# Optimization experiments

Hardware: AMD Instinct MI355X
Metric: run time of the kernel (lower is better)

The kernel has to match this reference:

```python
import jax, jax.numpy as jnp
import numpy as np

LEAK = 0.1
BN_EPS = 1e-3  # keras BatchNormalization default epsilon
H = 256        # LSTM hidden size


def _conv1d_same(x, k):
    # x: [B, T, Cin], k: [3, Cin, Cout] -> [B, T, Cout]
    return jax.lax.conv_general_dilated(x, k, (1,), 'SAME',
                                        dimension_numbers=('NWC', 'WIO', 'NWC'))


def _bn_leaky(x, gamma, beta, mean, var):
    y = (x - mean) * jax.lax.rsqrt(var + BN_EPS) * gamma + beta
    return jnp.where(y > 0, y, LEAK * y)


def _lstm_cell(x, h, c, W, U, b):
    # keras LSTMCell: gates ordered i, f, g(candidate), o
    z = x @ W + h @ U + b  # [B, 4H]
    i, f, g, o = jnp.split(z, 4, axis=-1)
    c_new = jax.nn.sigmoid(f) * c + jax.nn.sigmoid(i) * jnp.tanh(g)
    h_new = jax.nn.sigmoid(o) * jnp.tanh(c_new)
    return h_new, c_new


def setup_inputs() -> dict:
    key = jax.random.key(0)
    ks = jax.random.split(key, 16)
    B, T = 128, 1024
    d = {}
    d['imu'] = jax.random.normal(ks[0], (B, T, 6), dtype=jnp.float32)
    # conv encoder params (no bias)
    chans = [(6, 64), (64, 128), (128, 256)]
    for li, (cin, cout) in enumerate(chans, start=1):
        d[f'k{li}'] = jax.random.normal(ks[li], (3, cin, cout), jnp.float32) * (1.0 / np.sqrt(3 * cin))
        d[f'g{li}'] = jnp.ones((cout,), jnp.float32)
        d[f'b{li}'] = jnp.zeros((cout,), jnp.float32)
        d[f'm{li}'] = jax.random.normal(ks[li + 3], (cout,), jnp.float32) * 0.05
        d[f'v{li}'] = jax.random.uniform(ks[li + 6], (cout,), jnp.float32) + 0.5
    # stacked LSTM params (2 layers of 256 units)
    for li, kidx in [(1, 10), (2, 13)]:
        d[f'W{li}'] = jax.random.normal(ks[kidx], (H, 4 * H), jnp.float32) * (1.0 / np.sqrt(H))
        d[f'U{li}'] = jax.random.normal(ks[kidx + 1], (H, 4 * H), jnp.float32) * (1.0 / np.sqrt(H))
        d[f'bl{li}'] = jnp.zeros((4 * H,), jnp.float32)
    return d


def reference(imu, k1, g1, b1, m1, v1, k2, g2, b2, m2, v2, k3, g3, b3, m3, v3,
              W1, U1, bl1, W2, U2, bl2):
    # Conv1D-BN-LeakyReLU encoder (inference-mode BN, training=False)
    x = _bn_leaky(_conv1d_same(imu, k1), g1, b1, m1, v1)
    x = _bn_leaky(_conv1d_same(x, k2), g2, b2, m2, v2)
    x = _bn_leaky(_conv1d_same(x, k3), g3, b3, m3, v3)   # [B, T, 256]

    B = x.shape[0]
    init = tuple(jnp.zeros((B, H), x.dtype) for _ in range(4))  # h1, c1, h2, c2

    def step(carry, xt):
        h1, c1, h2, c2 = carry
        h1, c1 = _lstm_cell(xt, h1, c1, W1, U1, bl1)
        h2, c2 = _lstm_cell(h1, h2, c2, W2, U2, bl2)
        return (h1, c1, h2, c2), h2

    xs = jnp.swapaxes(x, 0, 1)           # [T, B, 256]
    _, ys = jax.lax.scan(step, init, xs)  # ys: [T, B, 256] top-layer outputs
    return jnp.mean(ys, axis=0)           # global average pool over time -> [B, 256]
```

## Files before the change

kernel.cpp:

```cpp
#include <hip/hip_runtime.h>
#include <hip/hip_bf16.h>

#define T_SEQ 1024
#define NB 128
#define HID 256
#define TEAM_BLK 32

typedef __attribute__((ext_vector_type(8))) short short8;
typedef __attribute__((ext_vector_type(4))) float f32x4;

__device__ __forceinline__ unsigned short f2bf(float f) {
  unsigned int u = __builtin_bit_cast(unsigned int, f);
  unsigned int r = (u + 0x7fffu + ((u >> 16) & 1u)) >> 16;
  return (unsigned short)r;
}

__device__ __forceinline__ float sigm(float x) { return 1.0f / (1.0f + expf(-x)); }

__device__ __forceinline__ int swz(int r, int k) {
  return (((r << 10) + (k << 1)) ^ ((r & 7) << 4)) >> 1;
}

__device__ __forceinline__ short8 ld_h16(const unsigned short* p) {
  unsigned long long lo = __hip_atomic_load((const unsigned long long*)p,
                                            __ATOMIC_RELAXED, __HIP_MEMORY_SCOPE_AGENT);
  unsigned long long hi = __hip_atomic_load((const unsigned long long*)(p + 4),
                                            __ATOMIC_RELAXED, __HIP_MEMORY_SCOPE_AGENT);
  union { unsigned long long q[2]; short8 v; } u;
  u.q[0] = lo; u.q[1] = hi;
  return u.v;
}
__device__ __forceinline__ void st_h(unsigned short* p, unsigned short v) {
  __hip_atomic_store(p, v, __ATOMIC_RELAXED, __HIP_MEMORY_SCOPE_AGENT);
}

__device__ __forceinline__ void team_arrive(unsigned int* flags, int bid, unsigned int val) {
  asm volatile("s_waitcnt vmcnt(0) lgkmcnt(0)" ::: "memory");
  if (threadIdx.x == 0)
    __hip_atomic_store(flags + bid, val, __ATOMIC_RELAXED, __HIP_MEMORY_SCOPE_AGENT);
}
__device__ __forceinline__ void team_wait(const unsigned int* flags, unsigned int val) {
  const unsigned int* p = flags + (threadIdx.x & 31);
  for (;;) {
    unsigned int v = __hip_atomic_load(p, __ATOMIC_RELAXED, __HIP_MEMORY_SCOPE_AGENT);
    if (__all(v >= val)) break;
    __builtin_amdgcn_s_sleep(1);
  }
  asm volatile("" ::: "memory");
}


__global__ void conv1_kernel(const float* __restrict__ imu, const float* __restrict__ k1,
                             const float* __restrict__ g1, const float* __restrict__ b1,
                             const float* __restrict__ m1, const float* __restrict__ v1,
                             float* __restrict__ y1) {
  int idx = blockIdx.x * 256 + threadIdx.x;
  int c = idx & 63;
  int t = (idx >> 6) & (T_SEQ - 1);
  int b = idx >> 16;
  float acc = 0.f;
#pragma unroll
  for (int dt = 0; dt < 3; ++dt) {
    int tt = t + dt - 1;
    if (tt >= 0 && tt < T_SEQ) {
      const float* ip = imu + ((size_t)b * T_SEQ + tt) * 6;
#pragma unroll
      for (int ci = 0; ci < 6; ++ci)
        acc += ip[ci] * k1[(dt * 6 + ci) * 64 + c];
    }
  }
  float sc = g1[c] * rsqrtf(v1[c] + 1e-3f);
  float y = (acc - m1[c]) * sc + b1[c];
  y1[idx] = y > 0.f ? y : 0.1f * y;
}

__global__ __launch_bounds__(128) void conv2_kernel(
    const float* __restrict__ y1, const float* __restrict__ k2,
    const float* __restrict__ g2, const float* __restrict__ b2,
    const float* __restrict__ m2, const float* __restrict__ v2,
    float* __restrict__ y2) {
  __shared__ float yt[18 * 64];
  const int b = blockIdx.x >> 6;
  const int t0 = (blockIdx.x & 63) << 4;
  for (int i = threadIdx.x; i < 18 * 64; i += 128) {
    int r = i >> 6, ci = i & 63;
    int tt = t0 - 1 + r;
    yt[i] = (tt >= 0 && tt < T_SEQ) ? y1[((size_t)b * T_SEQ + tt) * 64 + ci] : 0.f;
  }
  __syncthreads();
  const int c = threadIdx.x;
  float acc[16];
#pragma unroll
  for (int u = 0; u < 16; ++u) acc[u] = 0.f;
  for (int ci = 0; ci < 64; ++ci) {
    float w0 = k2[(0 * 64 + ci) * 128 + c];
    float w1 = k2[(1 * 64 + ci) * 128 + c];
    float w2 = k2[(2 * 64 + ci) * 128 + c];
    float rv[18];
#pragma unroll
    for (int r = 0; r < 18; ++r) rv[r] = yt[r * 64 + ci];
#pragma unroll
    for (int u = 0; u < 16; ++u)
      acc[u] += rv[u] * w0 + rv[u + 1] * w1 + rv[u + 2] * w2;
  }
  float sc = g2[c] * rsqrtf(v2[c] + 1e-3f);
  float sh = b2[c] - m2[c] * sc;
#pragma unroll
  for (int u = 0; u < 16; ++u) {
    float y = acc[u] * sc + sh;
    y2[((size_t)b * T_SEQ + (t0 + u)) * 128 + c] = y > 0.f ? y : 0.1f * y;
  }
}

__global__ __launch_bounds__(128) void conv3_kernel(
    const float* __restrict__ y2, const float* __restrict__ k3,
    const float* __restrict__ g3, const float* __restrict__ b3,
    const float* __restrict__ m3, const float* __restrict__ v3,
    unsigned short* __restrict__ x) {
  __shared__ float yt[18 * 128];
  const int b = blockIdx.x >> 6;
  const int t0 = (blockIdx.x & 63) << 4;
  for (int i = threadIdx.x; i < 18 * 128; i += 128) {
    int r = i >> 7, ci = i & 127;
    int tt = t0 - 1 + r;
    yt[i] = (tt >= 0 && tt < T_SEQ) ? y2[((size_t)b * T_SEQ + tt) * 128 + ci] : 0.f;
  }
  __syncthreads();
  const int c0 = threadIdx.x;
  float acc0[16], acc1[16];
#pragma unroll
  for (int u = 0; u < 16; ++u) { acc0[u] = 0.f; acc1[u] = 0.f; }
  for (int ci = 0; ci < 128; ++ci) {
    float w00 = k3[(0 * 128 + ci) * 256 + c0];
    float w01 = k3[(1 * 128 + ci) * 256 + c0];
    float w02 = k3[(2 * 128 + ci) * 256 + c0];
    float w10 = k3[(0 * 128 + ci) * 256 + c0 + 128];
    float w11 = k3[(1 * 128 + ci) * 256 + c0 + 128];
    float w12 = k3[(2 * 128 + ci) * 256 + c0 + 128];
    float rv[18];
#pragma unroll
    for (int r = 0; r < 18; ++r) rv[r] = yt[r * 128 + ci];
#pragma unroll
    for (int u = 0; u < 16; ++u) {
      acc0[u] += rv[u] * w00 + rv[u + 1] * w01 + rv[u + 2] * w02;
      acc1[u] += rv[u] * w10 + rv[u + 1] * w11 + rv[u + 2] * w12;
    }
  }
  float sca = g3[c0] * rsqrtf(v3[c0] + 1e-3f);
  float sha = b3[c0] - m3[c0] * sca;
  float scb = g3[c0 + 128] * rsqrtf(v3[c0 + 128] + 1e-3f);
  float shb = b3[c0 + 128] - m3[c0 + 128] * scb;
#pragma unroll
  for (int u = 0; u < 16; ++u) {
    float ya = acc0[u] * sca + sha;
    float yb = acc1[u] * scb + shb;
    ya = ya > 0.f ? ya : 0.1f * ya;
    yb = yb > 0.f ? yb : 0.1f * yb;
    size_t base = ((size_t)(t0 + u) * NB + b) * HID;
    x[base + c0] = f2bf(ya);
    x[base + c0 + 128] = f2bf(yb);
  }
}


__global__ __launch_bounds__(64) void lstm_kernel(
    const unsigned short* __restrict__ x,
    const float* __restrict__ W1, const float* __restrict__ U1, const float* __restrict__ bl1,
    const float* __restrict__ W2, const float* __restrict__ U2, const float* __restrict__ bl2,
    unsigned short* __restrict__ hbufs,
    unsigned int* __restrict__ bars,
    float* __restrict__ out) {
  __shared__ unsigned short wt[64 * 512];

  const int team = blockIdx.x >> 5;
  const int bid = blockIdx.x & 31;
  const bool is_l2 = bid >= 16;
  const int j0 = (bid & 15) << 4;
  const int lane = threadIdx.x;
  const int b0 = team << 4;

  const float* Wx = is_l2 ? W2 : W1;
  const float* Wh = is_l2 ? U2 : U1;
  const float* bl = is_l2 ? bl2 : bl1;

  {
    const int r = lane;
    const int col = ((r >> 4) << 8) + j0 + (r & 15);
    for (int k0 = 0; k0 < 256; k0 += 8) {
      short8 sx, sh;
#pragma unroll
      for (int u = 0; u < 8; ++u) {
        sx[u] = (short)f2bf(Wx[(size_t)(k0 + u) * 1024 + col]);
        sh[u] = (short)f2bf(Wh[(size_t)(k0 + u) * 1024 + col]);
      }
      *(short8*)&wt[swz(r, k0)] = sx;
      *(short8*)&wt[swz(r, 256 + k0)] = sh;
    }
  }

  const int lo4 = lane & 15;
  const int klo = (lane >> 4) << 3;

  float bias[4];
#pragma unroll
  for (int g = 0; g < 4; ++g) bias[g] = bl[(g << 8) + j0 + lo4];

  unsigned short* h1buf = hbufs + (size_t)team * 16384;
  unsigned short* h2buf = h1buf + 8192;
  unsigned int* flags = bars + team * 64;

  float cst[4] = {0.f, 0.f, 0.f, 0.f};
  float oacc[4] = {0.f, 0.f, 0.f, 0.f};
  f32x4 acc[4];

  if (!is_l2) {
#pragma unroll
    for (int g = 0; g < 4; ++g) acc[g] = (f32x4){bias[g], bias[g], bias[g], bias[g]};
    const unsigned short* xs = x + (size_t)(b0 + lo4) * HID;
#pragma unroll
    for (int kk = 0; kk < 8; ++kk) {
      short8 a = *(const short8*)(xs + kk * 32 + klo);
#pragma unroll
      for (int g = 0; g < 4; ++g)
        acc[g] = __builtin_amdgcn_mfma_f32_16x16x32_bf16(
            a, *(const short8*)&wt[swz((g << 4) + lo4, (kk << 5) + klo)], acc[g], 0, 0, 0);
    }
  }

  for (int ph = 0; ph <= T_SEQ; ++ph) {
    if (!is_l2) {
      if (ph < T_SEQ) {
        const unsigned short* hs = h1buf + ((ph + 1) & 1) * 4096 + lo4 * 256;
        short8 av[8];
#pragma unroll
        for (int kk = 0; kk < 8; ++kk) av[kk] = ld_h16(hs + kk * 32 + klo);
#pragma unroll
        for (int kk = 0; kk < 8; ++kk)
#pragma unroll
          for (int g = 0; g < 4; ++g)
            acc[g] = __builtin_amdgcn_mfma_f32_16x16x32_bf16(
                av[kk], *(const short8*)&wt[swz((g << 4) + lo4, 256 + (kk << 5) + klo)],
                acc[g], 0, 0, 0);
        unsigned short* dst = h1buf + (ph & 1) * 4096;
#pragma unroll
        for (int q = 0; q < 4; ++q) {
          float iv = acc[0][q], fv = acc[1][q], gv = acc[2][q], ov = acc[3][q];
          float cn = sigm(fv) * cst[q] + sigm(iv) * tanhf(gv);
          float hn = sigm(ov) * tanhf(cn);
          cst[q] = cn;
          int row = ((lane >> 4) << 2) + q;
          st_h(&dst[row * 256 + j0 + lo4], f2bf(hn));
        }
        team_arrive(flags, bid, (unsigned)(ph + 1));
        if (ph + 1 < T_SEQ) {
#pragma unroll
          for (int g = 0; g < 4; ++g) acc[g] = (f32x4){bias[g], bias[g], bias[g], bias[g]};
          const unsigned short* xs = x + ((size_t)(ph + 1) * NB + b0 + lo4) * HID;
#pragma unroll
          for (int kk = 0; kk < 8; ++kk) {
            short8 a = *(const short8*)(xs + kk * 32 + klo);
#pragma unroll
            for (int g = 0; g < 4; ++g)
              acc[g] = __builtin_amdgcn_mfma_f32_16x16x32_bf16(
                  a, *(const short8*)&wt[swz((g << 4) + lo4, (kk << 5) + klo)], acc[g], 0, 0, 0);
          }
          team_wait(flags, (unsigned)(ph + 1));
        }
      }
    } else {
      const int t = ph - 1;
      if (t >= 0) {
        const unsigned short* s0 = h1buf + (t & 1) * 4096 + lo4 * 256;
        const unsigned short* s1 = h2buf + ((t + 1) & 1) * 4096 + lo4 * 256;
        short8 a0[8], a1[8];
#pragma unroll
        for (int kk = 0; kk < 8; ++kk) a0[kk] = ld_h16(s0 + kk * 32 + klo);
#pragma unroll
        for (int kk = 0; kk < 8; ++kk) a1[kk] = ld_h16(s1 + kk * 32 + klo);
#pragma unroll
        for (int g = 0; g < 4; ++g) acc[g] = (f32x4){bias[g], bias[g], bias[g], bias[g]};
#pragma unroll
        for (int kk = 0; kk < 8; ++kk)
#pragma unroll
          for (int g = 0; g < 4; ++g)
            acc[g] = __builtin_amdgcn_mfma_f32_16x16x32_bf16(
                a0[kk], *(const short8*)&wt[swz((g << 4) + lo4, (kk << 5) + klo)],
                acc[g], 0, 0, 0);
#pragma unroll
        for (int kk = 0; kk < 8; ++kk)
#pragma unroll
          for (int g = 0; g < 4; ++g)
            acc[g] = __builtin_amdgcn_mfma_f32_16x16x32_bf16(
                a1[kk], *(const short8*)&wt[swz((g << 4) + lo4, 256 + (kk << 5) + klo)],
                acc[g], 0, 0, 0);
        unsigned short* dst = h2buf + (t & 1) * 4096;
#pragma unroll
        for (int q = 0; q < 4; ++q) {
          float iv = acc[0][q], fv = acc[1][q], gv = acc[2][q], ov = acc[3][q];
          float cn = sigm(fv) * cst[q] + sigm(iv) * tanhf(gv);
          float hn = sigm(ov) * tanhf(cn);
          cst[q] = cn;
          int row = ((lane >> 4) << 2) + q;
          st_h(&dst[row * 256 + j0 + lo4], f2bf(hn));
          oacc[q] += hn;
        }
      }
      if (ph < T_SEQ) {
        team_arrive(flags, bid, (unsigned)(ph + 1));
        team_wait(flags, (unsigned)(ph + 1));
      }
    }
  }

  if (is_l2) {
#pragma unroll
    for (int q = 0; q < 4; ++q) {
      int row = ((lane >> 4) << 2) + q;
      out[(size_t)(b0 + row) * HID + j0 + lo4] = oacc[q] * (1.0f / T_SEQ);
    }
  }
}


extern "C" void kernel_launch(void* const* d_in, const int* in_sizes, int n_in,
                              void* d_out, int out_size, void* d_ws, size_t ws_size,
                              hipStream_t stream) {
  const float* imu = (const float*)d_in[0];
  const float* k1 = (const float*)d_in[1];
  const float* g1 = (const float*)d_in[2];
  const float* b1 = (const float*)d_in[3];
  const float* m1 = (const float*)d_in[4];
  const float* v1 = (const float*)d_in[5];
  const float* k2 = (const float*)d_in[6];
  const float* g2 = (const float*)d_in[7];
  const float* b2 = (const float*)d_in[8];
  const float* m2 = (const float*)d_in[9];
  const float* v2 = (const float*)d_in[10];
  const float* k3 = (const float*)d_in[11];
  const float* g3 = (const float*)d_in[12];
  const float* b3 = (const float*)d_in[13];
  const float* m3 = (const float*)d_in[14];
  const float* v3 = (const float*)d_in[15];
  const float* W1 = (const float*)d_in[16];
  const float* U1 = (const float*)d_in[17];
  const float* bl1 = (const float*)d_in[18];
  const float* W2 = (const float*)d_in[19];
  const float* U2 = (const float*)d_in[20];
  const float* bl2 = (const float*)d_in[21];

  char* ws = (char*)d_ws;
  float* y2 = (float*)ws;
  float* y1 = (float*)(ws + (64u << 20));
  unsigned short* xq = (unsigned short*)(ws + (64u << 20));
  unsigned short* hbufs = (unsigned short*)(ws + (128u << 20));
  unsigned int* bars = (unsigned int*)(ws + (128u << 20) + (256u << 10));

  hipMemsetAsync(ws + (128u << 20), 0, (256u << 10) + 2048, stream);

  conv1_kernel<<<32768, 256, 0, stream>>>(imu, k1, g1, b1, m1, v1, y1);
  conv2_kernel<<<8192, 128, 0, stream>>>(y1, k2, g2, b2, m2, v2, y2);
  conv3_kernel<<<8192, 128, 0, stream>>>(y2, k3, g3, b3, m3, v3, xq);
  lstm_kernel<<<256, 64, 0, stream>>>(xq, W1, U1, bl1, W2, U2, bl2, hbufs, bars,
                                      (float*)d_out);
}
```

Measured before the change: 5.282 ms.

## Replace team barrier with pairwise flag waits, ring buffers, and register-resident weights

The all-to-all per-step barrier is replaced by per-producer progress tags: layer-1 blocks wait only on layer-1 peers (and on layer-2 three steps behind), and layer-2 blocks wait separately on layer-1 and layer-2 tags. The hidden-state buffers become 4-deep rings with a blocked layout, which lets layer 1 run ahead of layer 2. Weights move from LDS into registers (64 short8 per lane), the x-tile load is issued before publishing, and the spin sleep is removed. This aims to cut barrier latency and LDS reads on the serial recurrence, at the cost of very high register pressure (possible spills) and more aggressive polling.

After: 5.032 ms. 4.7% less time.

```diff
diff --git a/kernel.cpp b/kernel.cpp
--- a/kernel.cpp
+++ b/kernel.cpp
@@ -4,7 +4,7 @@
 #define T_SEQ 1024
 #define NB 128
 #define HID 256
-#define TEAM_BLK 32
+#define NEGINF_TGT (-(1 << 30))
 
 typedef __attribute__((ext_vector_type(8))) short short8;
 typedef __attribute__((ext_vector_type(4))) float f32x4;
@@ -16,10 +16,6 @@
 }
 
 __device__ __forceinline__ float sigm(float x) { return 1.0f / (1.0f + expf(-x)); }
-
-__device__ __forceinline__ int swz(int r, int k) {
-  return (((r << 10) + (k << 1)) ^ ((r & 7) << 4)) >> 1;
-}
 
 __device__ __forceinline__ short8 ld_h16(const unsigned short* p) {
   unsigned long long lo = __hip_atomic_load((const unsigned long long*)p,
@@ -34,17 +30,19 @@
   __hip_atomic_store(p, v, __ATOMIC_RELAXED, __HIP_MEMORY_SCOPE_AGENT);
 }
 
-__device__ __forceinline__ void team_arrive(unsigned int* flags, int bid, unsigned int val) {
+__device__ __forceinline__ void publish(int* tag, int val) {
   asm volatile("s_waitcnt vmcnt(0) lgkmcnt(0)" ::: "memory");
   if (threadIdx.x == 0)
-    __hip_atomic_store(flags + bid, val, __ATOMIC_RELAXED, __HIP_MEMORY_SCOPE_AGENT);
-}
-__device__ __forceinline__ void team_wait(const unsigned int* flags, unsigned int val) {
-  const unsigned int* p = flags + (threadIdx.x & 31);
+    __hip_atomic_store(tag, val, __ATOMIC_RELAXED, __HIP_MEMORY_SCOPE_AGENT);
+}
+
+__device__ __forceinline__ void wait_pair(const int* tags, int tgtA, int tgtB) {
+  const int l = threadIdx.x;
+  const int* p = tags + (l & 31);
+  const int tgt = (l & 16) ? tgtB : tgtA;
   for (;;) {
-    unsigned int v = __hip_atomic_load(p, __ATOMIC_RELAXED, __HIP_MEMORY_SCOPE_AGENT);
-    if (__all(v >= val)) break;
-    __builtin_amdgcn_s_sleep(1);
+    int v = __hip_atomic_load(p, __ATOMIC_RELAXED, __HIP_MEMORY_SCOPE_AGENT);
+    if (__all(v >= tgt)) break;
   }
   asm volatile("" ::: "memory");
 }
@@ -163,19 +161,18 @@
 }
 
 
-__global__ __launch_bounds__(64) void lstm_kernel(
+__global__ __launch_bounds__(64, 1) void lstm_kernel(
     const unsigned short* __restrict__ x,
     const float* __restrict__ W1, const float* __restrict__ U1, const float* __restrict__ bl1,
     const float* __restrict__ W2, const float* __restrict__ U2, const float* __restrict__ bl2,
     unsigned short* __restrict__ hbufs,
-    unsigned int* __restrict__ bars,
+    int* __restrict__ bars,
     float* __restrict__ out) {
-  __shared__ unsigned short wt[64 * 512];
-
   const int team = blockIdx.x >> 5;
   const int bid = blockIdx.x & 31;
   const bool is_l2 = bid >= 16;
-  const int j0 = (bid & 15) << 4;
+  const int pid = bid & 15;
+  const int j0 = pid << 4;
   const int lane = threadIdx.x;
   const int b0 = team << 4;
 
@@ -183,31 +180,37 @@
   const float* Wh = is_l2 ? U2 : U1;
   const float* bl = is_l2 ? bl2 : bl1;
 
-  {
-    const int r = lane;
-    const int col = ((r >> 4) << 8) + j0 + (r & 15);
-    for (int k0 = 0; k0 < 256; k0 += 8) {
-      short8 sx, sh;
-#pragma unroll
-      for (int u = 0; u < 8; ++u) {
-        sx[u] = (short)f2bf(Wx[(size_t)(k0 + u) * 1024 + col]);
-        sh[u] = (short)f2bf(Wh[(size_t)(k0 + u) * 1024 + col]);
-      }
-      *(short8*)&wt[swz(r, k0)] = sx;
-      *(short8*)&wt[swz(r, 256 + k0)] = sh;
-    }
-  }
-
   const int lo4 = lane & 15;
   const int klo = (lane >> 4) << 3;
 
+  short8 wB[2][8][4];
+  {
+    const float* Wsrc[2] = {Wx, Wh};
+#pragma unroll
+    for (int s = 0; s < 2; ++s)
+#pragma unroll
+      for (int kk = 0; kk < 8; ++kk)
+#pragma unroll
+        for (int g = 0; g < 4; ++g) {
+          short8 v;
+#pragma unroll
+          for (int e = 0; e < 8; ++e)
+            v[e] = (short)f2bf(Wsrc[s][(size_t)(kk * 32 + klo + e) * 1024 + (g << 8) + j0 + lo4]);
+          wB[s][kk][g] = v;
+        }
+  }
+
   float bias[4];
 #pragma unroll
   for (int g = 0; g < 4; ++g) bias[g] = bl[(g << 8) + j0 + lo4];
 
-  unsigned short* h1buf = hbufs + (size_t)team * 16384;
-  unsigned short* h2buf = h1buf + 8192;
-  unsigned int* flags = bars + team * 64;
+  unsigned short* h1b = hbufs + (size_t)team * 32768;
+  unsigned short* h2b = h1b + 16384;
+  int* tags = bars + team * 64;
+
+  const int cbase = ((klo >> 4) << 8) + (lo4 << 4) + (klo & 8);
+  const int row = ((lane >> 4) << 2);
+  const int stoff = pid * 256 + row * 16 + lo4;
 
   float cst[4] = {0.f, 0.f, 0.f, 0.f};
   float oacc[4] = {0.f, 0.f, 0.f, 0.f};
@@ -216,108 +219,99 @@
   if (!is_l2) {
 #pragma unroll
     for (int g = 0; g < 4; ++g) acc[g] = (f32x4){bias[g], bias[g], bias[g], bias[g]};
-    const unsigned short* xs = x + (size_t)(b0 + lo4) * HID;
-#pragma unroll
-    for (int kk = 0; kk < 8; ++kk) {
-      short8 a = *(const short8*)(xs + kk * 32 + klo);
-#pragma unroll
-      for (int g = 0; g < 4; ++g)
-        acc[g] = __builtin_amdgcn_mfma_f32_16x16x32_bf16(
-            a, *(const short8*)&wt[swz((g << 4) + lo4, (kk << 5) + klo)], acc[g], 0, 0, 0);
-    }
-  }
-
-  for (int ph = 0; ph <= T_SEQ; ++ph) {
-    if (!is_l2) {
-      if (ph < T_SEQ) {
-        const unsigned short* hs = h1buf + ((ph + 1) & 1) * 4096 + lo4 * 256;
+    {
+      const unsigned short* xs = x + (size_t)(b0 + lo4) * HID + klo;
+#pragma unroll
+      for (int kk = 0; kk < 8; ++kk) {
+        short8 a = *(const short8*)(xs + kk * 32);
+#pragma unroll
+        for (int g = 0; g < 4; ++g)
+          acc[g] = __builtin_amdgcn_mfma_f32_16x16x32_bf16(a, wB[0][kk][g], acc[g], 0, 0, 0);
+      }
+    }
+
+    for (int ph = 0; ph < T_SEQ; ++ph) {
+      wait_pair(tags, ph, ph - 3);
+      {
+        const unsigned short* src = h1b + ((ph + 3) & 3) * 4096 + cbase;
         short8 av[8];
 #pragma unroll
-        for (int kk = 0; kk < 8; ++kk) av[kk] = ld_h16(hs + kk * 32 + klo);
+        for (int kk = 0; kk < 8; ++kk) av[kk] = ld_h16(src + kk * 512);
 #pragma unroll
         for (int kk = 0; kk < 8; ++kk)
 #pragma unroll
           for (int g = 0; g < 4; ++g)
-            acc[g] = __builtin_amdgcn_mfma_f32_16x16x32_bf16(
-                av[kk], *(const short8*)&wt[swz((g << 4) + lo4, 256 + (kk << 5) + klo)],
-                acc[g], 0, 0, 0);
-        unsigned short* dst = h1buf + (ph & 1) * 4096;
-#pragma unroll
-        for (int q = 0; q < 4; ++q) {
-          float iv = acc[0][q], fv = acc[1][q], gv = acc[2][q], ov = acc[3][q];
-          float cn = sigm(fv) * cst[q] + sigm(iv) * tanhf(gv);
-          float hn = sigm(ov) * tanhf(cn);
-          cst[q] = cn;
-          int row = ((lane >> 4) << 2) + q;
-          st_h(&dst[row * 256 + j0 + lo4], f2bf(hn));
-        }
-        team_arrive(flags, bid, (unsigned)(ph + 1));
-        if (ph + 1 < T_SEQ) {
-#pragma unroll
-          for (int g = 0; g < 4; ++g) acc[g] = (f32x4){bias[g], bias[g], bias[g], bias[g]};
-          const unsigned short* xs = x + ((size_t)(ph + 1) * NB + b0 + lo4) * HID;
-#pragma unroll
-          for (int kk = 0; kk < 8; ++kk) {
-            short8 a = *(const short8*)(xs + kk * 32 + klo);
-#pragma unroll
-            for (int g = 0; g < 4; ++g)
-              acc[g] = __builtin_amdgcn_mfma_f32_16x16x32_bf16(
-                  a, *(const short8*)&wt[swz((g << 4) + lo4, (kk << 5) + klo)], acc[g], 0, 0, 0);
-          }
-          team_wait(flags, (unsigned)(ph + 1));
-        }
-      }
-    } else {
-      const int t = ph - 1;
-      if (t >= 0) {
-        const unsigned short* s0 = h1buf + (t & 1) * 4096 + lo4 * 256;
-        const unsigned short* s1 = h2buf + ((t + 1) & 1) * 4096 + lo4 * 256;
-        short8 a0[8], a1[8];
-#pragma unroll
-        for (int kk = 0; kk < 8; ++kk) a0[kk] = ld_h16(s0 + kk * 32 + klo);
-#pragma unroll
-        for (int kk = 0; kk < 8; ++kk) a1[kk] = ld_h16(s1 + kk * 32 + klo);
+            acc[g] = __builtin_amdgcn_mfma_f32_16x16x32_bf16(av[kk], wB[1][kk][g], acc[g], 0, 0, 0);
+      }
+      unsigned short* dst = h1b + (ph & 3) * 4096 + stoff;
+#pragma unroll
+      for (int q = 0; q < 4; ++q) {
+        float iv = acc[0][q], fv = acc[1][q], gv = acc[2][q], ov = acc[3][q];
+        float cn = sigm(fv) * cst[q] + sigm(iv) * tanhf(gv);
+        float hn = sigm(ov) * tanhf(cn);
+        cst[q] = cn;
+        st_h(dst + q * 16, f2bf(hn));
+      }
+      short8 xv[8];
+      if (ph + 1 < T_SEQ) {
+        const unsigned short* xs = x + ((size_t)(ph + 1) * NB + b0 + lo4) * HID + klo;
+#pragma unroll
+        for (int kk = 0; kk < 8; ++kk) xv[kk] = *(const short8*)(xs + kk * 32);
+      }
+      publish(&tags[pid], ph + 1);
+      if (ph + 1 < T_SEQ) {
 #pragma unroll
         for (int g = 0; g < 4; ++g) acc[g] = (f32x4){bias[g], bias[g], bias[g], bias[g]};
 #pragma unroll
         for (int kk = 0; kk < 8; ++kk)
 #pragma unroll
           for (int g = 0; g < 4; ++g)
-            acc[g] = __builtin_amdgcn_mfma_f32_16x16x32_bf16(
-                a0[kk], *(const short8*)&wt[swz((g << 4) + lo4, (kk << 5) + klo)],
-                acc[g], 0, 0, 0);
+            acc[g] = __builtin_amdgcn_mfma_f32_16x16x32_bf16(xv[kk], wB[0][kk][g], acc[g], 0, 0, 0);
+      }
+    }
+  } else {
+    for (int ph = 0; ph < T_SEQ; ++ph) {
+      wait_pair(tags, ph + 1, NEGINF_TGT);
+#pragma unroll
+      for (int g = 0; g < 4; ++g) acc[g] = (f32x4){bias[g], bias[g], bias[g], bias[g]};
+      {
+        const unsigned short* s1 = h1b + (ph & 3) * 4096 + cbase;
+        short8 av[8];
+#pragma unroll
+        for (int kk = 0; kk < 8; ++kk) av[kk] = ld_h16(s1 + kk * 512);
 #pragma unroll
         for (int kk = 0; kk < 8; ++kk)
 #pragma unroll
           for (int g = 0; g < 4; ++g)
-            acc[g] = __builtin_amdgcn_mfma_f32_16x16x32_bf16(
-                a1[kk], *(const short8*)&wt[swz((g << 4) + lo4, 256 + (kk << 5) + klo)],
-                acc[g], 0, 0, 0);
-        unsigned short* dst = h2buf + (t & 1) * 4096;
-#pragma unroll
-        for (int q = 0; q < 4; ++q) {
-          float iv = acc[0][q], fv = acc[1][q], gv = acc[2][q], ov = acc[3][q];
-          float cn = sigm(fv) * cst[q] + sigm(iv) * tanhf(gv);
-          float hn = sigm(ov) * tanhf(cn);
-          cst[q] = cn;
-          int row = ((lane >> 4) << 2) + q;
-          st_h(&dst[row * 256 + j0 + lo4], f2bf(hn));
-          oacc[q] += hn;
-        }
-      }
-      if (ph < T_SEQ) {
-        team_arrive(flags, bid, (unsigned)(ph + 1));
-        team_wait(flags, (unsigned)(ph + 1));
-      }
-    }
-  }
-
-  if (is_l2) {
-#pragma unroll
-    for (int q = 0; q < 4; ++q) {
-      int row = ((lane >> 4) << 2) + q;
-      out[(size_t)(b0 + row) * HID + j0 + lo4] = oacc[q] * (1.0f / T_SEQ);
-    }
+            acc[g] = __builtin_amdgcn_mfma_f32_16x16x32_bf16(av[kk], wB[0][kk][g], acc[g], 0, 0, 0);
+      }
+      wait_pair(tags, NEGINF_TGT, ph);
+      {
+        const unsigned short* s2 = h2b + ((ph + 3) & 3) * 4096 + cbase;
+        short8 av[8];
+#pragma unroll
+        for (int kk = 0; kk < 8; ++kk) av[kk] = ld_h16(s2 + kk * 512);
+#pragma unroll
+        for (int kk = 0; kk < 8; ++kk)
+#pragma unroll
+          for (int g = 0; g < 4; ++g)
+            acc[g] = __builtin_amdgcn_mfma_f32_16x16x32_bf16(av[kk], wB[1][kk][g], acc[g], 0, 0, 0);
+      }
+      unsigned short* dst = h2b + (ph & 3) * 4096 + stoff;
+#pragma unroll
+      for (int q = 0; q < 4; ++q) {
+        float iv = acc[0][q], fv = acc[1][q], gv = acc[2][q], ov = acc[3][q];
+        float cn = sigm(fv) * cst[q] + sigm(iv) * tanhf(gv);
+        float hn = sigm(ov) * tanhf(cn);
+        cst[q] = cn;
+        st_h(dst + q * 16, f2bf(hn));
+        oacc[q] += hn;
+      }
+      publish(&tags[16 + pid], ph + 1);
+    }
+#pragma unroll
+    for (int q = 0; q < 4; ++q)
+      out[(size_t)(b0 + row + q) * HID + j0 + lo4] = oacc[q] * (1.0f / T_SEQ);
   }
 }
 
@@ -353,9 +347,9 @@
   float* y1 = (float*)(ws + (64u << 20));
   unsigned short* xq = (unsigned short*)(ws + (64u << 20));
   unsigned short* hbufs = (unsigned short*)(ws + (128u << 20));
-  unsigned int* bars = (unsigned int*)(ws + (128u << 20) + (256u << 10));
-
-  hipMemsetAsync(ws + (128u << 20), 0, (256u << 10) + 2048, stream);
+  int* bars = (int*)(ws + (128u << 20) + (512u << 10));
+
+  hipMemsetAsync(ws + (128u << 20), 0, (512u << 10) + 2048, stream);
 
   conv1_kernel<<<32768, 256, 0, stream>>>(imu, k1, g1, b1, m1, v1, y1);
   conv2_kernel<<<8192, 128, 0, stream>>>(y1, k2, g2, b2, m2, v2, y2);
```
